# Optimization experiments

Measured on AMD Instinct MI355X. Metric: run time of the kernel, lower is better.

Reference implementation:

```python
import jax, jax.numpy as jnp
import numpy as np

NUM_HEADS = 12   # top-k = num_heads experts selected per token
SWITCHLOSS = 0.1
ZLOSS = 0.001


def setup_inputs() -> dict:
    key = jax.random.key(0)
    ks = jax.random.split(key, 8)
    B, N, C, E, D = 2, 2048, 768, 24, 64
    w = lambda k, shape: (jax.random.normal(k, shape, jnp.float32) * 0.02)
    return {
        "x": jax.random.normal(ks[0], (B, N, C), jnp.float32),
        "w_gate": w(ks[1], (C, E)),
        "W_in": w(ks[2], (E, C, D)),    # per-expert q projection
        "b_in": jnp.zeros((E, D), jnp.float32),
        "W_out": w(ks[3], (E, D, C)),   # per-expert output projection
        "b_out": jnp.zeros((E, C), jnp.float32),
        "W_kv": w(ks[4], (C, 2 * D)),   # shared single-head K/V
        "b_kv": jnp.zeros((2 * D,), jnp.float32),
    }


def reference(x, w_gate, W_in, b_in, W_out, b_out, W_kv, b_kv):
    B, N, C = x.shape
    E, _, D = W_in.shape
    H = NUM_HEADS
    scale = D ** -0.5

    xf = x.reshape(-1, C)                         # [T, C], T = B*N
    # --- top-k gating (k = num_heads) ---
    logits = xf @ w_gate                          # [T, E]
    probs = jax.nn.softmax(logits, axis=-1)
    top_p, idx = jax.lax.top_k(probs, H)          # [T, H]
    gates = top_p / (top_p.sum(-1, keepdims=True) + 1e-6)
    oh = jax.nn.one_hot(idx, E, dtype=x.dtype)    # [T, H, E]
    comb = oh * gates[..., None]                  # gated dispatch/combine weights

    # --- aux losses (switchloss + zloss; cvloss coeff = 0) ---
    dense_gates = comb.sum(1)                     # [T, E]
    freqs = (dense_gates > 0).astype(x.dtype).sum(0)
    p_sum = probs.sum(0)
    switch = E * jnp.sum((p_sum / p_sum.sum()) * (freqs / freqs.sum()))
    z = jnp.mean(jax.nn.logsumexp(logits, axis=1) ** 2)
    aux_loss = SWITCHLOSS * switch + ZLOSS * z

    # --- MoE map: per-token q via selected experts (no gate multiply) ---
    q_all = jnp.einsum('tc,ecd->ted', xf, W_in) + b_in     # [T, E, D]
    q = jnp.take_along_axis(q_all, idx[..., None], axis=1)  # [T, H, D]
    q = q.reshape(B, N, H, D)

    # --- shared-KV attention (multi-query style) ---
    kv = x @ W_kv + b_kv
    k, v = jnp.split(kv, 2, axis=-1)              # [B, N, D] each
    attn = jnp.einsum('bihd,bjd->bhij', q, k) * scale
    attn = jax.nn.softmax(attn, axis=-1)
    o = jnp.einsum('bhij,bjd->bihd', attn, v).reshape(-1, H, D)  # [T, H, D]

    # --- MoE reduce: gated combine through per-expert output projections ---
    xe = jnp.einsum('the,thd->ted', comb, o)      # [T, E, D] gated dispatch
    out = jnp.einsum('ted,edc->tc', xe, W_out) + jnp.einsum('the,ec->tc', comb, b_out)
    return out.reshape(B, N, C), aux_loss
```

## Files before the change

kernel.cpp:

```cpp
#include <hip/hip_runtime.h>
#include <hip/hip_bf16.h>

#define T_  4096
#define Bb  2
#define Nn  2048
#define Cc  768
#define Ee  24
#define Dd  64
#define Hh  12
#define KR  1568
#define KS  16
#define KC  48
#define NB2 1024
#define SCL 0.18033688f

typedef __attribute__((ext_vector_type(8))) short bf16x8;
typedef __attribute__((ext_vector_type(4))) short bf16x4;
typedef __attribute__((ext_vector_type(4))) float f32x4;

__device__ __forceinline__ unsigned short f2bf(float f) {
  union { float f; unsigned int i; } u; u.f = f;
  unsigned int r = u.i + 0x7FFFu + ((u.i >> 16) & 1u);
  return (unsigned short)(r >> 16);
}
__device__ __forceinline__ float bf2f(unsigned short s) {
  union { unsigned int i; float f; } u; u.i = ((unsigned int)s) << 16; return u.f;
}

__device__ __forceinline__ void gload16(const void* g, void* l) {
  __builtin_amdgcn_global_load_lds(
      (const __attribute__((address_space(1))) void*)g,
      (__attribute__((address_space(3))) void*)l, 16, 0, 0);
}

__global__ __launch_bounds__(256) void convert_all_kernel(
    const float* __restrict__ W_in, const float* __restrict__ W_out,
    const float* __restrict__ b_out, const float* __restrict__ W_kv,
    unsigned short* __restrict__ BqT, unsigned short* __restrict__ BrT,
    unsigned short* __restrict__ BkvT)
{
  __shared__ float ls[64 * 129];
  const int bid = blockIdx.x, tid = threadIdx.x;
  if (bid < 288) {
    const int e = bid / 12, c0 = (bid % 12) * 64;
    #pragma unroll
    for (int i = 0; i < 16; ++i) {
      int L = tid + i * 256, c = L >> 6, d = L & 63;
      ls[c * 65 + d] = W_in[(size_t)e * Cc * Dd + (size_t)(c0 + c) * Dd + d];
    }
    __syncthreads();
    #pragma unroll
    for (int i = 0; i < 16; ++i) {
      int L = tid + i * 256, d = L >> 6, c = L & 63;
      BqT[(size_t)(e * Dd + d) * Cc + c0 + c] = f2bf(ls[c * 65 + d]);
    }
  } else if (bid < 876) {
    const int i2 = bid - 288;
    const int k0 = (i2 / 12) * 32, n0 = (i2 % 12) * 64;
    #pragma unroll
    for (int i = 0; i < 8; ++i) {
      int L = tid + i * 256, k = L >> 6, n = L & 63;
      int kk = k0 + k;
      float v = (kk < 1536) ? W_out[(size_t)kk * Cc + n0 + n]
              : (kk < 1560) ? b_out[(size_t)(kk - 1536) * Cc + n0 + n] : 0.f;
      ls[k * 65 + n] = v;
    }
    __syncthreads();
    #pragma unroll
    for (int i = 0; i < 8; ++i) {
      int L = tid + i * 256, n = L >> 5, k = L & 31;
      BrT[(size_t)(n0 + n) * KR + k0 + k] = f2bf(ls[k * 65 + n]);
    }
  } else {
    const int c0 = (bid - 876) * 64;
    #pragma unroll
    for (int i = 0; i < 32; ++i) {
      int L = tid + i * 256, c = L >> 7, j = L & 127;
      ls[c * 129 + j] = W_kv[(size_t)(c0 + c) * 128 + j];
    }
    __syncthreads();
    #pragma unroll
    for (int i = 0; i < 32; ++i) {
      int L = tid + i * 256, j = L >> 6, c = L & 63;
      BkvT[(size_t)j * Cc + c0 + c] = f2bf(ls[c * 129 + j]);
    }
  }
}

template<int MODE, int BN>
__global__ __launch_bounds__(256) void gemm_bt_kernel(
    const unsigned short* __restrict__ A, const unsigned short* __restrict__ BT,
    const float* __restrict__ bias, const float* __restrict__ bias2,
    void* __restrict__ Cout, void* __restrict__ Cout2, void* __restrict__ Cout3,
    int K, int ldc)
{
  constexpr int BM = 64;
  constexpr int MI = 2;
  constexpr int NI = BN / 32;
  __shared__ __align__(16) unsigned short As[2][BM * 32];
  __shared__ __align__(16) unsigned short Bs[2][BN * 32];
  const int tid = threadIdx.x, w = tid >> 6, lane = tid & 63;
  const int quad = lane >> 4, nl = lane & 15;
  const int m0 = blockIdx.x * BM, n0 = blockIdx.y * BN;
  const int mw = (w & 1) * 32, nw = (w >> 1) * (BN / 2);

  f32x4 acc[MI][NI];
  #pragma unroll
  for (int i = 0; i < MI; ++i)
    #pragma unroll
    for (int j = 0; j < NI; ++j) acc[i][j] = (f32x4){0.f, 0.f, 0.f, 0.f};

  const int rlane = lane >> 2, col8 = (lane & 3) * 8;
  const unsigned short* a0 = A + (size_t)(m0 + w * 16 + rlane) * K + col8;
  const unsigned short* b0 =
      BT + (size_t)(n0 + (BN == 128 ? w * 32 : w * 16) + rlane) * K + col8;
  const unsigned short* b1 = b0 + (size_t)16 * K;

  auto STAGE = [&](int bi, int k0) {
    gload16(a0 + k0, &As[bi][(w * 16) * 32]);
    if (BN == 128) {
      gload16(b0 + k0, &Bs[bi][(w * 32) * 32]);
      gload16(b1 + k0, &Bs[bi][(w * 32 + 16) * 32]);
    } else {
      gload16(b0 + k0, &Bs[bi][(w * 16) * 32]);
    }
  };

  const int nt = K / 32;
  STAGE(0, 0);
  __syncthreads();
  for (int t = 0; t < nt; ++t) {
    const int cur = t & 1;
    if (t + 1 < nt) STAGE(cur ^ 1, (t + 1) * 32);

    const unsigned short* Ac = As[cur];
    const unsigned short* Bc = Bs[cur];
    bf16x8 af[MI], bfr[NI];
    #pragma unroll
    for (int mi = 0; mi < MI; ++mi)
      af[mi] = *(const bf16x8*)&Ac[(mw + mi * 16 + nl) * 32 + quad * 8];
    #pragma unroll
    for (int ni = 0; ni < NI; ++ni)
      bfr[ni] = *(const bf16x8*)&Bc[(nw + ni * 16 + nl) * 32 + quad * 8];
    #pragma unroll
    for (int mi = 0; mi < MI; ++mi)
      #pragma unroll
      for (int ni = 0; ni < NI; ++ni)
        acc[mi][ni] = __builtin_amdgcn_mfma_f32_16x16x32_bf16(
            af[mi], bfr[ni], acc[mi][ni], 0, 0, 0);

    __syncthreads();
  }

  #pragma unroll
  for (int mi = 0; mi < MI; ++mi) {
    int rowb = m0 + mw + mi * 16 + quad * 4;
    int bb = rowb >> 11, nn = rowb & (Nn - 1);
    #pragma unroll
    for (int ni = 0; ni < NI; ++ni) {
      int col = n0 + nw + ni * 16 + nl;
      if (MODE == 0) {
        #pragma unroll
        for (int reg = 0; reg < 4; ++reg)
          ((float*)Cout)[(size_t)(rowb + reg) * ldc + col] = acc[mi][ni][reg];
      } else {
        if (col < 1536) {
          float bv = bias[col];
          #pragma unroll
          for (int reg = 0; reg < 4; ++reg)
            ((unsigned short*)Cout)[(size_t)(rowb + reg) * 1536 + col] =
                f2bf((acc[mi][ni][reg] + bv) * SCL);
        } else {
          int c2 = col - 1536;
          float bv = bias2[c2];
          if (c2 < Dd) {
            #pragma unroll
            for (int reg = 0; reg < 4; ++reg)
              ((unsigned short*)Cout2)[((size_t)bb * Nn + nn + reg) * Dd + c2] =
                  f2bf(acc[mi][ni][reg] + bv);
          } else {
            int p6 = nn & 63;
            int np = (nn & ~63) | (p6 & 0x23)
                   | (((p6 >> 4) & 1) << 2) | (((p6 >> 2) & 3) << 3);
            ushort4 v;
            v.x = f2bf(acc[mi][ni][0] + bv);
            v.y = f2bf(acc[mi][ni][1] + bv);
            v.z = f2bf(acc[mi][ni][2] + bv);
            v.w = f2bf(acc[mi][ni][3] + bv);
            *(ushort4*)((unsigned short*)Cout3 +
                        ((size_t)bb * Dd + (c2 - Dd)) * Nn + np) = v;
          }
        }
      }
    }
  }
}

#define XPAD 52
__global__ __launch_bounds__(256) void gate1_kernel(
    const float* __restrict__ x, const float* __restrict__ wg,
    float* __restrict__ partial, unsigned short* __restrict__ xb)
{
  __shared__ __align__(16) float xs[256 * XPAD];
  __shared__ __align__(16) float wsT[Ee * KC];
  const int tid = threadIdx.x;
  const int t0 = blockIdx.x * 256;
  const int s = blockIdx.y, k0 = s * KC;

  #pragma unroll
  for (int i = 0; i < 12; ++i) {
    int f = tid + i * 256;
    int token = f / 12, j = f % 12;
    size_t gofs = (size_t)(t0 + token) * Cc + k0 + j * 4;
    float4 v = *(const float4*)&x[gofs];
    *(float4*)&xs[token * XPAD + j * 4] = v;
    ushort4 o;
    o.x = f2bf(v.x); o.y = f2bf(v.y); o.z = f2bf(v.z); o.w = f2bf(v.w);
    *(ushort4*)&xb[gofs] = o;
  }
  for (int i = tid; i < Ee * KC; i += 256)
    wsT[(i % Ee) * KC + i / Ee] = wg[k0 * Ee + i];
  __syncthreads();

  float xr[KC];
  #pragma unroll
  for (int kg = 0; kg < KC / 4; ++kg)
    *(float4*)&xr[kg * 4] = *(const float4*)&xs[tid * XPAD + kg * 4];

  float acc[Ee];
  #pragma unroll
  for (int e = 0; e < Ee; ++e) acc[e] = 0.f;
  #pragma unroll
  for (int e = 0; e < Ee; ++e) {
    #pragma unroll
    for (int kg = 0; kg < KC / 4; ++kg) {
      float4 wv = *(const float4*)&wsT[e * KC + kg * 4];
      acc[e] += xr[kg * 4 + 0] * wv.x + xr[kg * 4 + 1] * wv.y
              + xr[kg * 4 + 2] * wv.z + xr[kg * 4 + 3] * wv.w;
    }
  }

  float* dst = partial + ((size_t)(t0 + tid) * KS + s) * Ee;
  #pragma unroll
  for (int eg = 0; eg < Ee / 4; ++eg)
    *(float4*)&dst[eg * 4] = *(float4*)&acc[eg * 4];
}

__global__ __launch_bounds__(256) void gate2_kernel(
    const float* __restrict__ partial,
    int* __restrict__ idx, float* __restrict__ gate, float* __restrict__ bstats)
{
  __shared__ float xls[4][KS * Ee];
  __shared__ float sacc[49];
  const int tid = threadIdx.x;
  const int w = tid >> 6, lane = tid & 63;
  const int t = blockIdx.x * 4 + w;

  if (tid < 49) sacc[tid] = 0.f;

  const float* p = partial + (size_t)t * (KS * Ee);
  #pragma unroll
  for (int i = 0; i < 6; ++i) xls[w][lane + i * 64] = p[lane + i * 64];

  float logit = -1e30f;
  if (lane < Ee) {
    float acc = 0.f;
    #pragma unroll
    for (int s = 0; s < KS; ++s) acc += xls[w][s * Ee + lane];
    logit = acc;
  }
  float m = logit;
  for (int o = 32; o; o >>= 1) m = fmaxf(m, __shfl_xor(m, o));
  float pr = (lane < Ee) ? expf(logit - m) : 0.f;
  float s = pr;
  for (int o = 32; o; o >>= 1) s += __shfl_xor(s, o);
  float prob = pr / s;
  float lse = m + logf(s);

  bool sel = false;
  float my_p = 0.f; int my_e = -1;
  for (int h = 0; h < Hh; ++h) {
    float v = (lane < Ee && !sel) ? prob : -1.f;
    int ix = lane;
    for (int o = 32; o; o >>= 1) {
      float ov = __shfl_xor(v, o); int oi = __shfl_xor(ix, o);
      if (ov > v || (ov == v && oi < ix)) { v = ov; ix = oi; }
    }
    if (lane == ix) sel = true;
    if (lane == h) { my_p = v; my_e = ix; }
  }
  float gsum = (lane < Hh) ? my_p : 0.f;
  for (int o = 32; o; o >>= 1) gsum += __shfl_xor(gsum, o);
  if (lane < Hh) {
    idx[t * Hh + lane] = my_e;
    gate[t * Hh + lane] = my_p / (gsum + 1e-6f);
  }

  __syncthreads();
  if (lane < Ee) atomicAdd(&sacc[lane], prob);
  if (lane < Hh) atomicAdd(&sacc[24 + my_e], 1.0f);
  if (lane == 0) atomicAdd(&sacc[48], lse * lse);
  __syncthreads();
  if (tid < 49) bstats[(size_t)tid * NB2 + blockIdx.x] = sacc[tid];
}

__global__ __launch_bounds__(256, 3) void attn_kernel(
    const unsigned short* __restrict__ qallb, const int* __restrict__ idx,
    const unsigned short* __restrict__ kbuf, const unsigned short* __restrict__ vtbuf,
    float* __restrict__ opart, float* __restrict__ lpart)
{
  __shared__ __align__(16) unsigned short ksl[3][64 * 64];
  __shared__ __align__(16) unsigned short vtl[3][64 * 64];

  const int tid = threadIdx.x;
  const int w = tid >> 6, lane = tid & 63;
  const int quad = lane >> 4, nl = lane & 15;
  const int bh = blockIdx.y;
  const int b = bh / Hh, h = bh - b * Hh;
  const int qw = blockIdx.x * 64 + w * 16;

  const int tq = b * Nn + qw + nl;
  const int eq = idx[tq * Hh + h];
  const unsigned short* qrow = qallb + (size_t)tq * (Ee * Dd) + eq * Dd + quad * 8;
  const bf16x8 qB0 = *(const bf16x8*)(qrow);
  const bf16x8 qB1 = *(const bf16x8*)(qrow + 32);

  f32x4 acc[4];
  #pragma unroll
  for (int dg = 0; dg < 4; ++dg) acc[dg] = (f32x4){0.f, 0.f, 0.f, 0.f};
  float l = 0.f;

  const int sr  = lane >> 3;
  const int cbd = (lane & 7) ^ sr;
  const int xl  = nl & 7;
  const int ca0 = (quad ^ xl) * 8;
  const int ca1 = ((quad + 4) ^ xl) * 8;

  const unsigned short* kgbase =
      kbuf + ((size_t)b * Nn + w * 16 + sr) * Dd + cbd * 8;
  const unsigned short* vgbase =
      vtbuf + ((size_t)b * Dd + w * 16 + sr) * Nn + cbd * 8;

  auto STAGE = [&](int bi, int t) {
    const int j0 = t * 64;
    #pragma unroll
    for (int i = 0; i < 2; ++i) {
      gload16(kgbase + (size_t)(j0 + i * 8) * Dd, &ksl[bi][(w * 16 + i * 8) * 64]);
      gload16(vgbase + (size_t)(i * 8) * Nn + j0, &vtl[bi][(w * 16 + i * 8) * 64]);
    }
  };

  auto COMPUTE = [&](const unsigned short* ks_, const unsigned short* vt_) {
    __builtin_amdgcn_s_setprio(1);
    bf16x4 pf[4];
    #pragma unroll
    for (int kg = 0; kg < 4; ++kg) {
      const unsigned short* kr = ks_ + (kg * 16 + nl) * 64;
      bf16x8 a0 = *(const bf16x8*)(kr + ca0);
      bf16x8 a1 = *(const bf16x8*)(kr + ca1);
      f32x4 c = {0.f, 0.f, 0.f, 0.f};
      c = __builtin_amdgcn_mfma_f32_16x16x32_bf16(a0, qB0, c, 0, 0, 0);
      c = __builtin_amdgcn_mfma_f32_16x16x32_bf16(a1, qB1, c, 0, 0, 0);
      float p0 = __builtin_amdgcn_exp2f(c[0]);
      float p1 = __builtin_amdgcn_exp2f(c[1]);
      float p2 = __builtin_amdgcn_exp2f(c[2]);
      float p3 = __builtin_amdgcn_exp2f(c[3]);
      l += (p0 + p1) + (p2 + p3);
      union { __hip_bfloat162 h2[2]; bf16x4 v; } pk;
      pk.h2[0] = __float22bfloat162_rn(float2{p0, p1});
      pk.h2[1] = __float22bfloat162_rn(float2{p2, p3});
      pf[kg] = pk.v;
    }
    bf16x8 pb0 = __builtin_shufflevector(pf[0], pf[1], 0, 1, 2, 3, 4, 5, 6, 7);
    bf16x8 pb1 = __builtin_shufflevector(pf[2], pf[3], 0, 1, 2, 3, 4, 5, 6, 7);
    #pragma unroll
    for (int dg = 0; dg < 4; ++dg) {
      const unsigned short* vrow = vt_ + (dg * 16 + nl) * 64;
      bf16x8 v0 = *(const bf16x8*)(vrow + ca0);
      bf16x8 v1 = *(const bf16x8*)(vrow + ca1);
      acc[dg] = __builtin_amdgcn_mfma_f32_16x16x32_bf16(v0, pb0, acc[dg], 0, 0, 0);
      acc[dg] = __builtin_amdgcn_mfma_f32_16x16x32_bf16(v1, pb1, acc[dg], 0, 0, 0);
    }
    __builtin_amdgcn_s_setprio(0);
  };

  STAGE(0, 0);
  STAGE(1, 1);
  #pragma unroll 1
  for (int t = 0; t < 30; t += 3) {
    STAGE(2, t + 2);
    asm volatile("s_waitcnt vmcnt(8)" ::: "memory");
    __builtin_amdgcn_s_barrier();
    __builtin_amdgcn_sched_barrier(0);
    COMPUTE(ksl[0], vtl[0]);
    __builtin_amdgcn_sched_barrier(0);
    asm volatile("" ::: "memory");
    __builtin_amdgcn_s_barrier();

    STAGE(0, t + 3);
    asm volatile("s_waitcnt vmcnt(8)" ::: "memory");
    __builtin_amdgcn_s_barrier();
    __builtin_amdgcn_sched_barrier(0);
    COMPUTE(ksl[1], vtl[1]);
    __builtin_amdgcn_sched_barrier(0);
    asm volatile("" ::: "memory");
    __builtin_amdgcn_s_barrier();

    STAGE(1, t + 4);
    asm volatile("s_waitcnt vmcnt(8)" ::: "memory");
    __builtin_amdgcn_s_barrier();
    __builtin_amdgcn_sched_barrier(0);
    COMPUTE(ksl[2], vtl[2]);
    __builtin_amdgcn_sched_barrier(0);
    asm volatile("" ::: "memory");
    __builtin_amdgcn_s_barrier();
  }
  asm volatile("s_waitcnt vmcnt(4)" ::: "memory");
  __builtin_amdgcn_s_barrier();
  __builtin_amdgcn_sched_barrier(0);
  COMPUTE(ksl[0], vtl[0]);
  __builtin_amdgcn_sched_barrier(0);
  asm volatile("s_waitcnt vmcnt(0)" ::: "memory");
  __builtin_amdgcn_s_barrier();
  __builtin_amdgcn_sched_barrier(0);
  COMPUTE(ksl[1], vtl[1]);

  float lg = l;
  lg += __shfl_xor(lg, 16);
  lg += __shfl_xor(lg, 32);
  if (lane < 16)
    lpart[(size_t)bh * Nn + qw + nl] = lg;
  float* orow = opart + ((size_t)bh * Nn + qw + nl) * Dd + quad * 4;
  #pragma unroll
  for (int dg = 0; dg < 4; ++dg) {
    float4 o;
    o.x = acc[dg][0]; o.y = acc[dg][1];
    o.z = acc[dg][2]; o.w = acc[dg][3];
    *(float4*)(orow + dg * 16) = o;
  }
}

__global__ __launch_bounds__(256) void scatter_kernel(
    const float* __restrict__ opart, const float* __restrict__ lpart,
    const int* __restrict__ idx, const float* __restrict__ gate,
    unsigned short* __restrict__ xeg)
{
  __shared__ int   sel[Ee];
  __shared__ float glh[Hh];
  __shared__ float gg[Hh];
  const int t = blockIdx.x, b = t >> 11, nn = t & (Nn - 1);
  const int tid = threadIdx.x;
  if (tid < Ee) sel[tid] = -1;
  __syncthreads();
  if (tid < Hh) {
    int e = idx[t * Hh + tid];
    sel[e] = tid;
    float g = gate[t * Hh + tid];
    gg[tid] = g;
    size_t row = (size_t)(b * Hh + tid) * Nn + nn;
    glh[tid] = g / lpart[row];
  }
  __syncthreads();
  for (int c = tid; c < KR; c += 256) {
    float v = 0.f;
    if (c < 1536) {
      int e = c >> 6, h = sel[e];
      if (h >= 0) {
        size_t oofs = ((size_t)(b * Hh + h) * Nn + nn) * Dd + (c & 63);
        v = glh[h] * opart[oofs];
      }
    } else if (c < 1560) {
      int h = sel[c - 1536];
      if (h >= 0) v = gg[h];
    }
    xeg[(size_t)t * KR + c] = f2bf(v);
  }
}

__global__ __launch_bounds__(256) void aux1_kernel(
    const float* __restrict__ bstats, float* __restrict__ stats2)
{
  __shared__ float r[4];
  const int j = blockIdx.x, tid = threadIdx.x;
  float4 v = *(const float4*)&bstats[(size_t)j * NB2 + tid * 4];
  float s = (v.x + v.y) + (v.z + v.w);
  for (int o = 32; o; o >>= 1) s += __shfl_xor(s, o);
  if ((tid & 63) == 0) r[tid >> 6] = s;
  __syncthreads();
  if (tid == 0) stats2[j] = (r[0] + r[1]) + (r[2] + r[3]);
}

__global__ void aux2_kernel(const float* __restrict__ stats2,
                            float* __restrict__ out, int out_size)
{
  const int lane = threadIdx.x;
  float a = (lane < Ee) ? stats2[lane] : 0.f;
  float b = (lane < Ee) ? stats2[24 + lane] : 0.f;
  float pt = a, ft = b, sw = a * b;
  for (int o = 32; o; o >>= 1) {
    pt += __shfl_xor(pt, o); ft += __shfl_xor(ft, o); sw += __shfl_xor(sw, o);
  }
  if (lane == 0) {
    float sswitch = (float)Ee * sw / (pt * ft);
    float z = stats2[48] * (1.0f / (float)T_);
    out[out_size - 1] = 0.1f * sswitch + 0.001f * z;
  }
}

extern "C" void kernel_launch(void* const* d_in, const int* in_sizes, int n_in,
                              void* d_out, int out_size, void* d_ws, size_t ws_size,
                              hipStream_t stream)
{
  const float* x     = (const float*)d_in[0];
  const float* wg    = (const float*)d_in[1];
  const float* W_in  = (const float*)d_in[2];
  const float* b_in  = (const float*)d_in[3];
  const float* W_out = (const float*)d_in[4];
  const float* b_out = (const float*)d_in[5];
  const float* W_kv  = (const float*)d_in[6];
  const float* b_kv  = (const float*)d_in[7];
  float* out = (float*)d_out;

  char* ws = (char*)d_ws;
  size_t off = 0;
  auto carve = [&](size_t bytes) -> void* {
    void* p = ws + off;
    off = (off + bytes + 255) & ~(size_t)255;
    return p;
  };
  int*            idx    = (int*)           carve((size_t)T_ * Hh * 4);
  float*          gate   = (float*)         carve((size_t)T_ * Hh * 4);
  float*          bstats = (float*)         carve((size_t)49 * NB2 * 4);
  float*          stats2 = (float*)         carve(256);
  float*          lpart  = (float*)         carve((size_t)Bb * Hh * Nn * 4);
  float*          lgate  = (float*)         carve((size_t)T_ * KS * Ee * 4);
  unsigned short* xb     = (unsigned short*)carve((size_t)T_ * Cc * 2);
  unsigned short* BqkvT  = (unsigned short*)carve((size_t)(Ee * Dd + 128) * Cc * 2);
  unsigned short* BkvT   = BqkvT + (size_t)Ee * Dd * Cc;
  unsigned short* BrT    = (unsigned short*)carve((size_t)Cc * KR * 2);
  unsigned short* kbuf   = (unsigned short*)carve((size_t)T_ * Dd * 2);
  unsigned short* vtbuf  = (unsigned short*)carve((size_t)T_ * Dd * 2);
  unsigned short* qallb  = (unsigned short*)carve((size_t)T_ * Ee * Dd * 2);
  float*          opart  = (float*)         carve((size_t)Bb * Hh * Nn * Dd * 4);
  unsigned short* xeg    = (unsigned short*)carve((size_t)T_ * KR * 2);

  convert_all_kernel<<<888, 256, 0, stream>>>(
      W_in, W_out, b_out, W_kv, BqkvT, BrT, BkvT);

  gate1_kernel<<<dim3(T_ / 256, KS), 256, 0, stream>>>(x, wg, lgate, xb);
  gate2_kernel<<<NB2, 256, 0, stream>>>(lgate, idx, gate, bstats);

  gemm_bt_kernel<1, 64><<<dim3(T_ / 64, 26), 256, 0, stream>>>(
      xb, BqkvT, b_in, b_kv, qallb, kbuf, vtbuf, Cc, 1536);

  attn_kernel<<<dim3(Nn / 64, Bb * Hh), 256, 0, stream>>>(
      qallb, idx, kbuf, vtbuf, opart, lpart);

  scatter_kernel<<<T_, 256, 0, stream>>>(opart, lpart, idx, gate, xeg);

  gemm_bt_kernel<0, 64><<<dim3(T_ / 64, Cc / 64), 256, 0, stream>>>(
      xeg, BrT, nullptr, nullptr, out, nullptr, nullptr, KR, Cc);

  aux1_kernel<<<49, 256, 0, stream>>>(bstats, stats2);
  aux2_kernel<<<1, 64, 0, stream>>>(stats2, out, out_size);
}
```

Before: 203.1 us.

## Fuse gated scatter into the output-projection GEMM A-tile construction

Removes the scatter kernel that materialised a dense bf16 [T, KR] gated dispatch matrix. The reduce GEMM now builds its A tiles on the fly from opart, lpart, idx and gate, using per-block shared tables for expert selection and scaling, and writes them into LDS. This saves a large intermediate write and read plus one launch. In exchange, each of the 12 column blocks recomputes the A tiles and rereads fp32 opart, and A-tile production is now synchronous register work rather than async global-to-LDS loads.

```diff
diff --git a/kernel.cpp b/kernel.cpp
--- a/kernel.cpp
+++ b/kernel.cpp
@@ -23,9 +23,6 @@
   unsigned int r = u.i + 0x7FFFu + ((u.i >> 16) & 1u);
   return (unsigned short)(r >> 16);
 }
-__device__ __forceinline__ float bf2f(unsigned short s) {
-  union { unsigned int i; float f; } u; u.i = ((unsigned int)s) << 16; return u.f;
-}
 
 __device__ __forceinline__ void gload16(const void* g, void* l) {
   __builtin_amdgcn_global_load_lds(
@@ -87,22 +84,19 @@
   }
 }
 
-template<int MODE, int BN>
-__global__ __launch_bounds__(256) void gemm_bt_kernel(
+__global__ __launch_bounds__(256) void gemm_qkv_kernel(
     const unsigned short* __restrict__ A, const unsigned short* __restrict__ BT,
     const float* __restrict__ bias, const float* __restrict__ bias2,
-    void* __restrict__ Cout, void* __restrict__ Cout2, void* __restrict__ Cout3,
-    int K, int ldc)
-{
-  constexpr int BM = 64;
-  constexpr int MI = 2;
-  constexpr int NI = BN / 32;
+    unsigned short* __restrict__ Cout, unsigned short* __restrict__ Cout2,
+    unsigned short* __restrict__ Cout3, int K)
+{
+  constexpr int BM = 64, BN = 64, MI = 2, NI = 2;
   __shared__ __align__(16) unsigned short As[2][BM * 32];
   __shared__ __align__(16) unsigned short Bs[2][BN * 32];
   const int tid = threadIdx.x, w = tid >> 6, lane = tid & 63;
   const int quad = lane >> 4, nl = lane & 15;
   const int m0 = blockIdx.x * BM, n0 = blockIdx.y * BN;
-  const int mw = (w & 1) * 32, nw = (w >> 1) * (BN / 2);
+  const int mw = (w & 1) * 32, nw = (w >> 1) * 32;
 
   f32x4 acc[MI][NI];
   #pragma unroll
@@ -112,18 +106,11 @@
 
   const int rlane = lane >> 2, col8 = (lane & 3) * 8;
   const unsigned short* a0 = A + (size_t)(m0 + w * 16 + rlane) * K + col8;
-  const unsigned short* b0 =
-      BT + (size_t)(n0 + (BN == 128 ? w * 32 : w * 16) + rlane) * K + col8;
-  const unsigned short* b1 = b0 + (size_t)16 * K;
+  const unsigned short* b0 = BT + (size_t)(n0 + w * 16 + rlane) * K + col8;
 
   auto STAGE = [&](int bi, int k0) {
     gload16(a0 + k0, &As[bi][(w * 16) * 32]);
-    if (BN == 128) {
-      gload16(b0 + k0, &Bs[bi][(w * 32) * 32]);
-      gload16(b1 + k0, &Bs[bi][(w * 32 + 16) * 32]);
-    } else {
-      gload16(b0 + k0, &Bs[bi][(w * 16) * 32]);
-    }
+    gload16(b0 + k0, &Bs[bi][(w * 16) * 32]);
   };
 
   const int nt = K / 32;
@@ -159,39 +146,155 @@
     #pragma unroll
     for (int ni = 0; ni < NI; ++ni) {
       int col = n0 + nw + ni * 16 + nl;
-      if (MODE == 0) {
+      if (col < 1536) {
+        float bv = bias[col];
         #pragma unroll
         for (int reg = 0; reg < 4; ++reg)
-          ((float*)Cout)[(size_t)(rowb + reg) * ldc + col] = acc[mi][ni][reg];
+          Cout[(size_t)(rowb + reg) * 1536 + col] =
+              f2bf((acc[mi][ni][reg] + bv) * SCL);
       } else {
-        if (col < 1536) {
-          float bv = bias[col];
+        int c2 = col - 1536;
+        float bv = bias2[c2];
+        if (c2 < Dd) {
           #pragma unroll
           for (int reg = 0; reg < 4; ++reg)
-            ((unsigned short*)Cout)[(size_t)(rowb + reg) * 1536 + col] =
-                f2bf((acc[mi][ni][reg] + bv) * SCL);
+            Cout2[((size_t)bb * Nn + nn + reg) * Dd + c2] =
+                f2bf(acc[mi][ni][reg] + bv);
         } else {
-          int c2 = col - 1536;
-          float bv = bias2[c2];
-          if (c2 < Dd) {
-            #pragma unroll
-            for (int reg = 0; reg < 4; ++reg)
-              ((unsigned short*)Cout2)[((size_t)bb * Nn + nn + reg) * Dd + c2] =
-                  f2bf(acc[mi][ni][reg] + bv);
-          } else {
-            int p6 = nn & 63;
-            int np = (nn & ~63) | (p6 & 0x23)
-                   | (((p6 >> 4) & 1) << 2) | (((p6 >> 2) & 3) << 3);
-            ushort4 v;
-            v.x = f2bf(acc[mi][ni][0] + bv);
-            v.y = f2bf(acc[mi][ni][1] + bv);
-            v.z = f2bf(acc[mi][ni][2] + bv);
-            v.w = f2bf(acc[mi][ni][3] + bv);
-            *(ushort4*)((unsigned short*)Cout3 +
-                        ((size_t)bb * Dd + (c2 - Dd)) * Nn + np) = v;
-          }
+          int p6 = nn & 63;
+          int np = (nn & ~63) | (p6 & 0x23)
+                 | (((p6 >> 4) & 1) << 2) | (((p6 >> 2) & 3) << 3);
+          ushort4 v;
+          v.x = f2bf(acc[mi][ni][0] + bv);
+          v.y = f2bf(acc[mi][ni][1] + bv);
+          v.z = f2bf(acc[mi][ni][2] + bv);
+          v.w = f2bf(acc[mi][ni][3] + bv);
+          *(ushort4*)(Cout3 + ((size_t)bb * Dd + (c2 - Dd)) * Nn + np) = v;
         }
       }
+    }
+  }
+}
+
+__global__ __launch_bounds__(256) void gemm_reduce_kernel(
+    const float* __restrict__ opart, const float* __restrict__ lpart,
+    const int* __restrict__ idx, const float* __restrict__ gate,
+    const unsigned short* __restrict__ BT, float* __restrict__ out)
+{
+  constexpr int BM = 64, BN = 64, MI = 2, NI = 2;
+  __shared__ __align__(16) unsigned short As[2][BM * 32];
+  __shared__ __align__(16) unsigned short Bs[2][BN * 32];
+  __shared__ signed char sel8[64][Ee];
+  __shared__ float glh_l[64][Hh];
+  __shared__ float gg_l[64][Hh];
+
+  const int tid = threadIdx.x, w = tid >> 6, lane = tid & 63;
+  const int quad = lane >> 4, nl = lane & 15;
+  const int m0 = blockIdx.x * BM, n0 = blockIdx.y * BN;
+  const int mw = (w & 1) * 32, nw = (w >> 1) * 32;
+
+  for (int i = tid; i < 64 * Ee; i += 256) ((signed char*)sel8)[i] = -1;
+  __syncthreads();
+  for (int i = tid; i < 64 * Hh; i += 256) {
+    int tl = i / Hh, hh = i - tl * Hh;
+    int token = m0 + tl;
+    int e = idx[token * Hh + hh];
+    sel8[tl][e] = (signed char)hh;
+    float g = gate[token * Hh + hh];
+    gg_l[tl][hh] = g;
+    int bb = token >> 11, nn = token & (Nn - 1);
+    glh_l[tl][hh] = g / lpart[(size_t)(bb * Hh + hh) * Nn + nn];
+  }
+
+  f32x4 acc[MI][NI];
+  #pragma unroll
+  for (int i = 0; i < MI; ++i)
+    #pragma unroll
+    for (int j = 0; j < NI; ++j) acc[i][j] = (f32x4){0.f, 0.f, 0.f, 0.f};
+
+  const int rlane = lane >> 2, col8 = (lane & 3) * 8;
+  const int rl = w * 16 + rlane;
+  const int token = m0 + rl;
+  const int bb = token >> 11, nn = token & (Nn - 1);
+  const unsigned short* b0 = BT + (size_t)(n0 + w * 16 + rlane) * KR + col8;
+
+  auto MAKE_A = [&](int k0) -> bf16x8 {
+    bf16x8 r = (bf16x8){0, 0, 0, 0, 0, 0, 0, 0};
+    const int c0 = k0 + col8;
+    if (c0 < 1536) {
+      int e = c0 >> 6;
+      int h = sel8[rl][e];
+      if (h >= 0) {
+        float sc = glh_l[rl][h];
+        const float* op = opart +
+            ((size_t)(bb * Hh + h) * Nn + nn) * Dd + (c0 & 63);
+        float4 v0 = *(const float4*)op;
+        float4 v1 = *(const float4*)(op + 4);
+        union { __hip_bfloat162 h2[4]; bf16x8 v; } pk;
+        pk.h2[0] = __float22bfloat162_rn(float2{sc * v0.x, sc * v0.y});
+        pk.h2[1] = __float22bfloat162_rn(float2{sc * v0.z, sc * v0.w});
+        pk.h2[2] = __float22bfloat162_rn(float2{sc * v1.x, sc * v1.y});
+        pk.h2[3] = __float22bfloat162_rn(float2{sc * v1.z, sc * v1.w});
+        r = pk.v;
+      }
+    } else {
+      #pragma unroll
+      for (int j = 0; j < 8; ++j) {
+        int c = c0 + j;
+        if (c < 1560) {
+          int h = sel8[rl][c - 1536];
+          if (h >= 0) ((unsigned short*)&r)[j] = f2bf(gg_l[rl][h]);
+        }
+      }
+    }
+    return r;
+  };
+
+  const int nt = KR / 32;
+  __syncthreads();
+  bf16x8 a_first = MAKE_A(0);
+  *(bf16x8*)&As[0][rl * 32 + col8] = a_first;
+  gload16(b0, &Bs[0][(w * 16) * 32]);
+  __syncthreads();
+
+  for (int t = 0; t < nt; ++t) {
+    const int cur = t & 1;
+    bf16x8 an;
+    if (t + 1 < nt) {
+      an = MAKE_A((t + 1) * 32);
+      gload16(b0 + (t + 1) * 32, &Bs[cur ^ 1][(w * 16) * 32]);
+    }
+
+    const unsigned short* Ac = As[cur];
+    const unsigned short* Bc = Bs[cur];
+    bf16x8 af[MI], bfr[NI];
+    #pragma unroll
+    for (int mi = 0; mi < MI; ++mi)
+      af[mi] = *(const bf16x8*)&Ac[(mw + mi * 16 + nl) * 32 + quad * 8];
+    #pragma unroll
+    for (int ni = 0; ni < NI; ++ni)
+      bfr[ni] = *(const bf16x8*)&Bc[(nw + ni * 16 + nl) * 32 + quad * 8];
+    #pragma unroll
+    for (int mi = 0; mi < MI; ++mi)
+      #pragma unroll
+      for (int ni = 0; ni < NI; ++ni)
+        acc[mi][ni] = __builtin_amdgcn_mfma_f32_16x16x32_bf16(
+            af[mi], bfr[ni], acc[mi][ni], 0, 0, 0);
+
+    if (t + 1 < nt)
+      *(bf16x8*)&As[cur ^ 1][rl * 32 + col8] = an;
+    __syncthreads();
+  }
+
+  #pragma unroll
+  for (int mi = 0; mi < MI; ++mi) {
+    int rowb = m0 + mw + mi * 16 + quad * 4;
+    #pragma unroll
+    for (int ni = 0; ni < NI; ++ni) {
+      int col = n0 + nw + ni * 16 + nl;
+      #pragma unroll
+      for (int reg = 0; reg < 4; ++reg)
+        out[(size_t)(rowb + reg) * Cc + col] = acc[mi][ni][reg];
     }
   }
 }
@@ -437,43 +540,6 @@
     o.x = acc[dg][0]; o.y = acc[dg][1];
     o.z = acc[dg][2]; o.w = acc[dg][3];
     *(float4*)(orow + dg * 16) = o;
-  }
-}
-
-__global__ __launch_bounds__(256) void scatter_kernel(
-    const float* __restrict__ opart, const float* __restrict__ lpart,
-    const int* __restrict__ idx, const float* __restrict__ gate,
-    unsigned short* __restrict__ xeg)
-{
-  __shared__ int   sel[Ee];
-  __shared__ float glh[Hh];
-  __shared__ float gg[Hh];
-  const int t = blockIdx.x, b = t >> 11, nn = t & (Nn - 1);
-  const int tid = threadIdx.x;
-  if (tid < Ee) sel[tid] = -1;
-  __syncthreads();
-  if (tid < Hh) {
-    int e = idx[t * Hh + tid];
-    sel[e] = tid;
-    float g = gate[t * Hh + tid];
-    gg[tid] = g;
-    size_t row = (size_t)(b * Hh + tid) * Nn + nn;
-    glh[tid] = g / lpart[row];
-  }
-  __syncthreads();
-  for (int c = tid; c < KR; c += 256) {
-    float v = 0.f;
-    if (c < 1536) {
-      int e = c >> 6, h = sel[e];
-      if (h >= 0) {
-        size_t oofs = ((size_t)(b * Hh + h) * Nn + nn) * Dd + (c & 63);
-        v = glh[h] * opart[oofs];
-      }
-    } else if (c < 1560) {
-      int h = sel[c - 1536];
-      if (h >= 0) v = gg[h];
-    }
-    xeg[(size_t)t * KR + c] = f2bf(v);
   }
 }
 
@@ -542,7 +608,6 @@
   unsigned short* vtbuf  = (unsigned short*)carve((size_t)T_ * Dd * 2);
   unsigned short* qallb  = (unsigned short*)carve((size_t)T_ * Ee * Dd * 2);
   float*          opart  = (float*)         carve((size_t)Bb * Hh * Nn * Dd * 4);
-  unsigned short* xeg    = (unsigned short*)carve((size_t)T_ * KR * 2);
 
   convert_all_kernel<<<888, 256, 0, stream>>>(
       W_in, W_out, b_out, W_kv, BqkvT, BrT, BkvT);
@@ -550,16 +615,14 @@
   gate1_kernel<<<dim3(T_ / 256, KS), 256, 0, stream>>>(x, wg, lgate, xb);
   gate2_kernel<<<NB2, 256, 0, stream>>>(lgate, idx, gate, bstats);
 
-  gemm_bt_kernel<1, 64><<<dim3(T_ / 64, 26), 256, 0, stream>>>(
-      xb, BqkvT, b_in, b_kv, qallb, kbuf, vtbuf, Cc, 1536);
+  gemm_qkv_kernel<<<dim3(T_ / 64, 26), 256, 0, stream>>>(
+      xb, BqkvT, b_in, b_kv, qallb, kbuf, vtbuf, Cc);
 
   attn_kernel<<<dim3(Nn / 64, Bb * Hh), 256, 0, stream>>>(
       qallb, idx, kbuf, vtbuf, opart, lpart);
 
-  scatter_kernel<<<T_, 256, 0, stream>>>(opart, lpart, idx, gate, xeg);
-
-  gemm_bt_kernel<0, 64><<<dim3(T_ / 64, Cc / 64), 256, 0, stream>>>(
-      xeg, BrT, nullptr, nullptr, out, nullptr, nullptr, KR, Cc);
+  gemm_reduce_kernel<<<dim3(T_ / 64, Cc / 64), 256, 0, stream>>>(
+      opart, lpart, idx, gate, BrT, out);
 
   aux1_kernel<<<49, 256, 0, stream>>>(bstats, stats2);
   aux2_kernel<<<1, 64, 0, stream>>>(stats2, out, out_size);
```

After: 215.8 us. 6.2% more time.
